# Kernel tuning notes

Hardware: AMD Instinct MI355X
Metric: run time of the kernel (lower is better)

## Reference

```python
import jax, jax.numpy as jnp
import numpy as np

L, B = 1024, 64
VALID_FRAC = 0.9  # fraction of residues with nonzero (observed) coordinates in y


def setup_inputs() -> dict:
    key = jax.random.key(0)
    kx, ky = jax.random.split(key)
    x = jax.random.normal(kx, (L, B, 3), dtype=jnp.float32)
    y = jax.random.normal(ky, (L, B, 3), dtype=jnp.float32)
    # zero out trailing residues in y so the dynamic mask (co.sum() != 0) is exercised
    valid = (jnp.arange(L) < int(VALID_FRAC * L))[:, None, None]
    y = y * valid.astype(jnp.float32)
    return {"x": x, "y": y}


def _masked_pair_dist(pts, pair_mask):
    # pts: [B, L, 3]; pair_mask: [B, L, L] (False on diagonal and on padded rows/cols)
    sq = jnp.sum(pts * pts, axis=-1)                                   # [B, L]
    d2 = sq[:, :, None] + sq[:, None, :] - 2.0 * jnp.einsum('bld,bmd->blm', pts, pts)
    d2 = jnp.maximum(d2, 0.0)                                          # relu, matches F.relu
    safe = jnp.where(pair_mask, d2, 1.0)                               # keep sqrt grad finite
    return jnp.where(pair_mask, jnp.sqrt(safe), 0.0)


def reference(x, y):
    # x, y: [L, B, 3] -> permute to [B, L, 3] as in the torch module
    xb = jnp.transpose(x, (1, 0, 2))
    yb = jnp.transpose(y, (1, 0, 2))
    Bn, Ln = xb.shape[0], xb.shape[1]
    # mask: residues of y whose coordinate sum is nonzero (index_select in original)
    mask = (jnp.sum(yb, axis=-1) != 0)                                 # [B, L]
    off_diag = ~jnp.eye(Ln, dtype=bool)
    pair_mask = mask[:, :, None] & mask[:, None, :] & off_diag         # [B, L, L]
    xd = _masked_pair_dist(xb, pair_mask)
    yd = _masked_pair_dist(yb, pair_mask)
    D = yd - xd                                                        # [B, L, L]
    per_batch = jnp.sqrt(jnp.sum(D * D, axis=(1, 2)))                  # Frobenius norm per batch
    denom = (Ln ** 2 / 2 - Ln) ** 0.5                                  # x.size(1)**2/2 - x.size(1)
    out = jnp.sum(per_batch) / denom / Bn
    return out.reshape(1)
```

## Files before the change

### kernel.cpp

```cpp
#include <hip/hip_runtime.h>
#include <math.h>

#define Lp 1024
#define Bp 64
#define Tt 128
#define NTILE 8
#define NPAIR 36

typedef float v2 __attribute__((ext_vector_type(2)));
static __device__ __forceinline__ v2 splat2(float s) { v2 r; r.x = s; r.y = s; return r; }

__global__ __launch_bounds__(256) void drmsd_main(
    const float* __restrict__ x, const float* __restrict__ y,
    float* __restrict__ partials)
{
    __shared__ __align__(16) float xsx[2][Tt], xsy[2][Tt], xsz[2][Tt];
    __shared__ __align__(16) float ysx[2][Tt], ysy[2][Tt], ysz[2][Tt];
    __shared__ __align__(16) float ms[2][Tt];
    __shared__ float red[4];

    const int b = blockIdx.x;
    const int p = blockIdx.y;

    int ti = 0, base = 0;
    while (p >= base + (NTILE - ti)) { base += (NTILE - ti); ++ti; }
    const int tj = ti + (p - base);

    const int t = threadIdx.x;

    {
        const int r     = t & (Tt - 1);
        const int which = t >> 7;
        const int tile  = which ? tj : ti;
        const int row   = tile * Tt + r;
        const float* px = x + (size_t)row * (Bp * 3) + (size_t)b * 3;
        const float* py = y + (size_t)row * (Bp * 3) + (size_t)b * 3;
        const float x0 = px[0], x1 = px[1], x2 = px[2];
        const float y0 = py[0], y1 = py[1], y2 = py[2];
        xsx[which][r] = x0; xsy[which][r] = x1; xsz[which][r] = x2;
        ysx[which][r] = y0; ysy[which][r] = y1; ysz[which][r] = y2;
        ms[which][r]  = ((y0 + y1 + y2) != 0.0f) ? 1.0f : 0.0f;
    }
    __syncthreads();

    const int jsl2 = (t & 15) << 1;
    const int rg   = t >> 4;

    float total = 0.0f;
    const v2 neg2 = splat2(-2.0f);

#pragma unroll
    for (int half = 0; half < 2; ++half) {
        const int i0 = half * 64 + rg * 4;
        const float4 v_xx = *(const float4*)&xsx[0][i0];
        const float4 v_xy = *(const float4*)&xsy[0][i0];
        const float4 v_xz = *(const float4*)&xsz[0][i0];
        const float4 v_yx = *(const float4*)&ysx[0][i0];
        const float4 v_yy = *(const float4*)&ysy[0][i0];
        const float4 v_yz = *(const float4*)&ysz[0][i0];
        const float4 v_mi = *(const float4*)&ms[0][i0];
        const float xix[4] = { v_xx.x, v_xx.y, v_xx.z, v_xx.w };
        const float xiy[4] = { v_xy.x, v_xy.y, v_xy.z, v_xy.w };
        const float xiz[4] = { v_xz.x, v_xz.y, v_xz.z, v_xz.w };
        const float yix[4] = { v_yx.x, v_yx.y, v_yx.z, v_yx.w };
        const float yiy[4] = { v_yy.x, v_yy.y, v_yy.z, v_yy.w };
        const float yiz[4] = { v_yz.x, v_yz.y, v_yz.z, v_yz.w };
        const float mir[4] = { v_mi.x, v_mi.y, v_mi.z, v_mi.w };

        v2 acc[4];
#pragma unroll
        for (int r = 0; r < 4; ++r) acc[r] = splat2(0.0f);

#pragma unroll
        for (int jj = 0; jj < 4; ++jj) {
            const int j0 = jj * 32 + jsl2;
            const v2 xjx = *(const v2*)&xsx[1][j0];
            const v2 xjy = *(const v2*)&xsy[1][j0];
            const v2 xjz = *(const v2*)&xsz[1][j0];
            const v2 yjx = *(const v2*)&ysx[1][j0];
            const v2 yjy = *(const v2*)&ysy[1][j0];
            const v2 yjz = *(const v2*)&ysz[1][j0];
            const v2 mj  = *(const v2*)&ms[1][j0];
#pragma unroll
            for (int r = 0; r < 4; ++r) {
                const v2 ax = splat2(xix[r]) - xjx;
                const v2 ay = splat2(xiy[r]) - xjy;
                const v2 az = splat2(xiz[r]) - xjz;
                const v2 d2x = ax * ax + ay * ay + az * az;
                const v2 bx = splat2(yix[r]) - yjx;
                const v2 by = splat2(yiy[r]) - yjy;
                const v2 bz = splat2(yiz[r]) - yjz;
                const v2 d2y = bx * bx + by * by + bz * bz;
                const v2 pr = d2x * d2y;
                v2 sq;
                sq.x = __builtin_amdgcn_sqrtf(pr.x);
                sq.y = __builtin_amdgcn_sqrtf(pr.y);
                const v2 u = (d2x + d2y) + neg2 * sq;
                acc[r] = mj * u + acc[r];
            }
        }
#pragma unroll
        for (int r = 0; r < 4; ++r)
            total = fmaf(acc[r].x + acc[r].y, mir[r], total);
    }

#pragma unroll
    for (int off = 32; off > 0; off >>= 1)
        total += __shfl_down(total, off, 64);
    const int wave = t >> 6;
    if ((t & 63) == 0) red[wave] = total;
    __syncthreads();
    if (t == 0) {
        float s = red[0] + red[1] + red[2] + red[3];
        if (ti != tj) s *= 2.0f;
        partials[(size_t)p * Bp + b] = s;
    }
}

__global__ __launch_bounds__(256) void drmsd_final(
    const float* __restrict__ partials, float* __restrict__ out)
{
    __shared__ float sums[256];
    const int t    = threadIdx.x;
    const int lane = t & 63;
    const int q    = t >> 6;
    float s = 0.0f;
#pragma unroll
    for (int k = 0; k < 9; ++k) {
        const int pidx = q * 9 + k;
        s += partials[(size_t)pidx * Bp + lane];
    }
    sums[t] = s;
    __syncthreads();
    if (t < 64) {
        float v = sums[t] + sums[t + 64] + sums[t + 128] + sums[t + 192];
        float pb = sqrtf(v);
#pragma unroll
        for (int off = 32; off > 0; off >>= 1)
            pb += __shfl_down(pb, off, 64);
        if (t == 0) {
            const double denom = sqrt((double)Lp * (double)Lp / 2.0 - (double)Lp);
            out[0] = (float)((double)pb / denom / (double)Bp);
        }
    }
}

extern "C" void kernel_launch(void* const* d_in, const int* in_sizes, int n_in,
                              void* d_out, int out_size, void* d_ws, size_t ws_size,
                              hipStream_t stream) {
    const float* x = (const float*)d_in[0];
    const float* y = (const float*)d_in[1];
    float* out      = (float*)d_out;
    float* partials = (float*)d_ws;

    dim3 grid(Bp, NPAIR);
    drmsd_main<<<grid, 256, 0, stream>>>(x, y, partials);
    drmsd_final<<<1, 256, 0, stream>>>(partials, out);
}
```

Measured before the change: 69.86 us.

## Fuse final reduction via atomic counter and skip empty 32-row masked chunks

Merges the final reduction kernel into the main kernel: the last block to finish, found with an atomic counter, sums the partials and writes the output. A memset now resets the counter before each launch. Each block also builds per-32-row validity bitmasks in shared memory, so warps skip i-chunks and j-chunks whose rows are all masked out. The per-thread j work widens from 2 to 4 lanes, which removes the two-half loop. This adds atomics and a fence to every block in exchange for dropping one kernel launch and the work on masked rows.

```diff
diff --git a/kernel.cpp b/kernel.cpp
--- a/kernel.cpp
+++ b/kernel.cpp
@@ -6,18 +6,25 @@
 #define Tt 128
 #define NTILE 8
 #define NPAIR 36
+#define NBLK (Bp * NPAIR)
 
-typedef float v2 __attribute__((ext_vector_type(2)));
-static __device__ __forceinline__ v2 splat2(float s) { v2 r; r.x = s; r.y = s; return r; }
+typedef float v4f __attribute__((ext_vector_type(4)));
+static __device__ __forceinline__ v4f splat4(float s) {
+    v4f r; r.x = s; r.y = s; r.z = s; r.w = s; return r;
+}
 
-__global__ __launch_bounds__(256) void drmsd_main(
+__global__ __launch_bounds__(256) void drmsd_fused(
     const float* __restrict__ x, const float* __restrict__ y,
-    float* __restrict__ partials)
+    float* __restrict__ partials, unsigned* __restrict__ counter,
+    float* __restrict__ out)
 {
     __shared__ __align__(16) float xsx[2][Tt], xsy[2][Tt], xsz[2][Tt];
     __shared__ __align__(16) float ysx[2][Tt], ysy[2][Tt], ysz[2][Tt];
     __shared__ __align__(16) float ms[2][Tt];
+    __shared__ unsigned vflags[2];
     __shared__ float red[4];
+    __shared__ int   lastFlag;
+    __shared__ float sums[256];
 
     const int b = blockIdx.x;
     const int p = blockIdx.y;
@@ -27,6 +34,8 @@
     const int tj = ti + (p - base);
 
     const int t = threadIdx.x;
+    if (t < 2) vflags[t] = 0u;
+    __syncthreads();
 
     {
         const int r     = t & (Tt - 1);
@@ -39,19 +48,23 @@
         const float y0 = py[0], y1 = py[1], y2 = py[2];
         xsx[which][r] = x0; xsy[which][r] = x1; xsz[which][r] = x2;
         ysx[which][r] = y0; ysy[which][r] = y1; ysz[which][r] = y2;
-        ms[which][r]  = ((y0 + y1 + y2) != 0.0f) ? 1.0f : 0.0f;
+        const bool valid = ((y0 + y1 + y2) != 0.0f);
+        ms[which][r] = valid ? 1.0f : 0.0f;
+        if (valid) atomicOr(&vflags[which], 1u << (r >> 5));
     }
     __syncthreads();
 
-    const int jsl2 = (t & 15) << 1;
-    const int rg   = t >> 4;
+    const unsigned imask = vflags[0];
+    const unsigned jmask = vflags[1];
+
+    const int jsl = (t & 7) << 2;
+    const int rg  = t >> 3;
+    const int i0  = rg << 2;
+    const int wv  = t >> 6;
 
     float total = 0.0f;
-    const v2 neg2 = splat2(-2.0f);
 
-#pragma unroll
-    for (int half = 0; half < 2; ++half) {
-        const int i0 = half * 64 + rg * 4;
+    if (imask & (1u << wv)) {
         const float4 v_xx = *(const float4*)&xsx[0][i0];
         const float4 v_xy = *(const float4*)&xsy[0][i0];
         const float4 v_xz = *(const float4*)&xsz[0][i0];
@@ -67,80 +80,85 @@
         const float yiz[4] = { v_yz.x, v_yz.y, v_yz.z, v_yz.w };
         const float mir[4] = { v_mi.x, v_mi.y, v_mi.z, v_mi.w };
 
-        v2 acc[4];
+        v4f acc[4];
 #pragma unroll
-        for (int r = 0; r < 4; ++r) acc[r] = splat2(0.0f);
+        for (int r = 0; r < 4; ++r) acc[r] = splat4(0.0f);
+
+        const v4f neg2 = splat4(-2.0f);
 
 #pragma unroll
         for (int jj = 0; jj < 4; ++jj) {
-            const int j0 = jj * 32 + jsl2;
-            const v2 xjx = *(const v2*)&xsx[1][j0];
-            const v2 xjy = *(const v2*)&xsy[1][j0];
-            const v2 xjz = *(const v2*)&xsz[1][j0];
-            const v2 yjx = *(const v2*)&ysx[1][j0];
-            const v2 yjy = *(const v2*)&ysy[1][j0];
-            const v2 yjz = *(const v2*)&ysz[1][j0];
-            const v2 mj  = *(const v2*)&ms[1][j0];
+            if (!(jmask & (1u << jj))) continue;
+            const int j0 = jj * 32 + jsl;
+            const v4f xjx = *(const v4f*)&xsx[1][j0];
+            const v4f xjy = *(const v4f*)&xsy[1][j0];
+            const v4f xjz = *(const v4f*)&xsz[1][j0];
+            const v4f yjx = *(const v4f*)&ysx[1][j0];
+            const v4f yjy = *(const v4f*)&ysy[1][j0];
+            const v4f yjz = *(const v4f*)&ysz[1][j0];
+            const v4f mj  = *(const v4f*)&ms[1][j0];
 #pragma unroll
             for (int r = 0; r < 4; ++r) {
-                const v2 ax = splat2(xix[r]) - xjx;
-                const v2 ay = splat2(xiy[r]) - xjy;
-                const v2 az = splat2(xiz[r]) - xjz;
-                const v2 d2x = ax * ax + ay * ay + az * az;
-                const v2 bx = splat2(yix[r]) - yjx;
-                const v2 by = splat2(yiy[r]) - yjy;
-                const v2 bz = splat2(yiz[r]) - yjz;
-                const v2 d2y = bx * bx + by * by + bz * bz;
-                const v2 pr = d2x * d2y;
-                v2 sq;
+                const v4f ax = splat4(xix[r]) - xjx;
+                const v4f ay = splat4(xiy[r]) - xjy;
+                const v4f az = splat4(xiz[r]) - xjz;
+                const v4f d2x = ax * ax + ay * ay + az * az;
+                const v4f bx = splat4(yix[r]) - yjx;
+                const v4f by = splat4(yiy[r]) - yjy;
+                const v4f bz = splat4(yiz[r]) - yjz;
+                const v4f d2y = bx * bx + by * by + bz * bz;
+                const v4f pr = d2x * d2y;
+                v4f sq;
                 sq.x = __builtin_amdgcn_sqrtf(pr.x);
                 sq.y = __builtin_amdgcn_sqrtf(pr.y);
-                const v2 u = (d2x + d2y) + neg2 * sq;
+                sq.z = __builtin_amdgcn_sqrtf(pr.z);
+                sq.w = __builtin_amdgcn_sqrtf(pr.w);
+                const v4f u = (d2x + d2y) + neg2 * sq;
                 acc[r] = mj * u + acc[r];
             }
         }
 #pragma unroll
         for (int r = 0; r < 4; ++r)
-            total = fmaf(acc[r].x + acc[r].y, mir[r], total);
+            total = fmaf(acc[r].x + acc[r].y + acc[r].z + acc[r].w, mir[r], total);
     }
 
 #pragma unroll
     for (int off = 32; off > 0; off >>= 1)
         total += __shfl_down(total, off, 64);
-    const int wave = t >> 6;
-    if ((t & 63) == 0) red[wave] = total;
+    if ((t & 63) == 0) red[wv] = total;
     __syncthreads();
     if (t == 0) {
         float s = red[0] + red[1] + red[2] + red[3];
         if (ti != tj) s *= 2.0f;
         partials[(size_t)p * Bp + b] = s;
+        __threadfence();
+        const unsigned old = atomicAdd(counter, 1u);
+        lastFlag = (old == NBLK - 1) ? 1 : 0;
     }
-}
+    __syncthreads();
 
-__global__ __launch_bounds__(256) void drmsd_final(
-    const float* __restrict__ partials, float* __restrict__ out)
-{
-    __shared__ float sums[256];
-    const int t    = threadIdx.x;
-    const int lane = t & 63;
-    const int q    = t >> 6;
-    float s = 0.0f;
+    if (lastFlag) {
+        __threadfence();
+        const int lane = t & 63;
+        const int q    = t >> 6;
+        float s = 0.0f;
 #pragma unroll
-    for (int k = 0; k < 9; ++k) {
-        const int pidx = q * 9 + k;
-        s += partials[(size_t)pidx * Bp + lane];
-    }
-    sums[t] = s;
-    __syncthreads();
-    if (t < 64) {
-        float v = sums[t] + sums[t + 64] + sums[t + 128] + sums[t + 192];
-        float pb = sqrtf(v);
+        for (int k = 0; k < 9; ++k) {
+            const int pidx = q * 9 + k;
+            s += partials[(size_t)pidx * Bp + lane];
+        }
+        sums[t] = s;
+        __syncthreads();
+        if (t < 64) {
+            float v = sums[t] + sums[t + 64] + sums[t + 128] + sums[t + 192];
+            float pb = sqrtf(v);
 #pragma unroll
-        for (int off = 32; off > 0; off >>= 1)
-            pb += __shfl_down(pb, off, 64);
-        if (t == 0) {
-            const double denom = sqrt((double)Lp * (double)Lp / 2.0 - (double)Lp);
-            out[0] = (float)((double)pb / denom / (double)Bp);
+            for (int off = 32; off > 0; off >>= 1)
+                pb += __shfl_down(pb, off, 64);
+            if (t == 0) {
+                const double denom = sqrt((double)Lp * (double)Lp / 2.0 - (double)Lp);
+                out[0] = (float)((double)pb / denom / (double)Bp);
+            }
         }
     }
 }
@@ -152,8 +170,9 @@
     const float* y = (const float*)d_in[1];
     float* out      = (float*)d_out;
     float* partials = (float*)d_ws;
+    unsigned* counter = (unsigned*)((char*)d_ws + 9216);
 
+    hipMemsetAsync(counter, 0, sizeof(unsigned), stream);
     dim3 grid(Bp, NPAIR);
-    drmsd_main<<<grid, 256, 0, stream>>>(x, y, partials);
-    drmsd_final<<<1, 256, 0, stream>>>(partials, out);
+    drmsd_fused<<<grid, 256, 0, stream>>>(x, y, partials, counter, out);
 }
```

Result: slower. 104.5 us (+49.6%).
